# Kernel tuning notes

Hardware: AMD Instinct MI355X
Metric: run time of the kernel (lower is better)

## Reference

```python
import jax, jax.numpy as jnp
import numpy as np

B, N, Q, M, OUT = 8192, 512, 6, 1024, 256
QUANTILE_COEFFS = np.array([-3.0, -0.834, -0.248, 0.248, 0.834], dtype=np.float32)


def setup_inputs() -> dict:
    key = jax.random.key(0)
    k1, k2, k3, k4, k5, k6, k7 = jax.random.split(key, 7)
    x = jax.random.normal(k1, (B, N), dtype=jnp.float32)
    beta = jnp.zeros((N,), dtype=jnp.float32)
    gamma = jnp.ones((N,), dtype=jnp.float32)
    w = jax.random.normal(k2, (N * Q + M, OUT), dtype=jnp.float32)
    biases = jax.random.normal(k3, (1,), dtype=jnp.float32)
    # chosen_index rows: (count, n1, q1, n2, q2); n-indices in [0,N), q-indices in [0,Q)
    cnt = jnp.arange(M, dtype=jnp.int64)[:, None]
    n1 = jax.random.randint(k4, (M, 1), 0, N)
    q1 = jax.random.randint(k5, (M, 1), 0, Q)
    n2 = jax.random.randint(k6, (M, 1), 0, N)
    q2 = jax.random.randint(k7, (M, 1), 0, Q)
    chosen_index = jnp.concatenate([cnt, n1, q1, n2, q2], axis=1).astype(jnp.int64)
    return {"x": x, "beta": beta, "gamma": gamma, "w": w, "biases": biases,
            "chosen_index": chosen_index}


def reference(x, beta, gamma, w, biases, chosen_index):
    # Batch norm (EMA with decay=0.5 after register+update collapses to batch stats)
    mean = jnp.mean(x, axis=0)                      # (N,)
    var = jnp.var(x, axis=0)                        # (N,) biased, like unbiased=False
    normed = gamma * (x - mean) / jnp.sqrt(var + 0.001) + beta   # (B, N)
    # Maxout: base ReLU + 5 quantile-thresholded branches
    coeffs = jnp.asarray(QUANTILE_COEFFS)           # (5,)
    quant = coeffs[:, None] * var[None, :] + mean[None, :]       # (5, N)
    base = jnp.maximum(0.0, normed)[None]                        # (1, B, N)
    branches = jnp.maximum(0.0, normed[None] - quant[:, None, :] * gamma + beta)  # (5, B, N)
    stacked = jnp.concatenate([base, branches], axis=0)          # (Q, B, N)
    max_x = jnp.transpose(stacked, (1, 2, 0))                    # (B, N, Q)
    # Minout (test mode): per-row gather of two (n,q) coords, elementwise min
    n1, q1 = chosen_index[:, 1], chosen_index[:, 2]
    n2, q2 = chosen_index[:, 3], chosen_index[:, 4]
    D1 = max_x[:, n1, q1]                                        # (B, M)
    D2 = max_x[:, n2, q2]                                        # (B, M)
    min_x = jnp.minimum(D1, D2)                                  # (B, M)
    feat = jnp.concatenate([max_x.reshape(x.shape[0], -1), min_x], axis=1)  # (B, N*Q+M)
    output = feat @ w + biases                                   # (B, OUT)
    return output
```

## Files before the change

kernel.cpp:

```cpp
#include <hip/hip_runtime.h>
#include <stdint.h>

typedef unsigned int uint32;
typedef unsigned short u16;
typedef __attribute__((ext_vector_type(8))) short bf16x8;
typedef __attribute__((ext_vector_type(4))) float f32x4;

#define WS_SCALE 0
#define WS_SHIFT 512
#define WS_SUBQ  1024
#define WS_SHSUB 4096
#define WS_PSUM  8192
#define WS_PSQ   (8192+65536)
#define WRT_OFF  (1u<<20)
#define AMIN_OFF (3u<<20)
#define PART_OFF (19u<<20)

__device__ __forceinline__ u16 f2bf(float f){
  uint32 u; __builtin_memcpy(&u,&f,4);
  u = u + 0x7fffu + ((u>>16)&1u);
  return (u16)(u>>16);
}
__device__ __forceinline__ float bf2f(u16 b){
  uint32 u = ((uint32)b)<<16; float f; __builtin_memcpy(&f,&u,4); return f;
}
__device__ __forceinline__ uint32 pk2(float a, float b){
  return (uint32)f2bf(a) | ((uint32)f2bf(b)<<16);
}
__device__ __forceinline__ void gll16(u16* lds, const u16* g){
  __builtin_amdgcn_global_load_lds((const __attribute__((address_space(1))) uint32*)g,
                                   (__attribute__((address_space(3))) uint32*)lds, 16, 0, 0);
}

__global__ __launch_bounds__(512) void k_pre(const float* __restrict__ x,
                                             const float* __restrict__ w,
                                             float* __restrict__ ws,
                                             u16* __restrict__ wrT){
  int b = blockIdx.x, t = threadIdx.x;
  if (b < 128){
    const float* xp = x + (size_t)b*64*512 + t;
    float sum = 0.f, sq = 0.f;
    #pragma unroll 8
    for (int r=0; r<64; ++r){ float v = xp[(size_t)r*512]; sum += v; sq += v*v; }
    ws[WS_PSUM + b*512 + t] = sum;
    ws[WS_PSQ  + b*512 + t] = sq;
  } else {
    int c2 = b - 128;
    int o = t & 255, half = t >> 8;
    int swzrow = (o >> 1) & 3;
    u16* dst = wrT + (size_t)c2*8192 + o*32;
    #pragma unroll
    for (int gi=0; gi<2; ++gi){
      int g = half*2 + gi;
      union { bf16x8 v; u16 h[8]; } R;
      #pragma unroll
      for (int e=0; e<8; ++e){
        int k = g*8 + e;
        int sk;
        if (c2 < 96) sk = ((c2 & 15)*32 + k)*6 + (c2 >> 4);
        else         sk = 3072 + (c2 - 96)*32 + k;
        R.h[e] = f2bf(w[(size_t)sk*256 + o]);
      }
      *(bf16x8*)(dst + ((g ^ swzrow)*8)) = R.v;
    }
  }
}

__global__ __launch_bounds__(512) void k_stats_final(const float* __restrict__ beta,
                                                     const float* __restrict__ gamma,
                                                     float* __restrict__ ws){
  int n = threadIdx.x;
  float sum = 0.f, sq = 0.f;
  #pragma unroll 8
  for (int s2=0; s2<128; ++s2){ sum += ws[WS_PSUM + s2*512 + n]; sq += ws[WS_PSQ + s2*512 + n]; }
  float mean = sum * (1.0f/8192.0f);
  float var  = sq  * (1.0f/8192.0f) - mean*mean;
  float g = gamma[n], b = beta[n];
  float inv = 1.0f / sqrtf(var + 0.001f);
  float scale = g * inv;
  float shift = b - mean*scale;
  ws[WS_SCALE + n] = scale;
  ws[WS_SHIFT + n] = shift;
  const float QC[5] = {-3.0f, -0.834f, -0.248f, 0.248f, 0.834f};
  ws[WS_SUBQ  + n] = 0.f;
  ws[WS_SHSUB + n] = shift;
  #pragma unroll
  for (int c=0; c<5; ++c){
    float sub = (QC[c]*var + mean)*g - b;
    ws[WS_SUBQ  + (c+1)*512 + n] = sub;
    ws[WS_SHSUB + (c+1)*512 + n] = shift - sub;
  }
}

__global__ __launch_bounds__(256) void k_minfeat(const float* __restrict__ x,
                                                 const float* __restrict__ ws,
                                                 const int* __restrict__ ci,
                                                 u16* __restrict__ amin){
  __shared__ float nrm[8][512];
  __shared__ uint32 tnn[1024];
  __shared__ float ts1[1024];
  __shared__ float ts2[1024];
  int t = threadIdx.x;
  int b0 = blockIdx.x * 8;
  #pragma unroll
  for (int ii=0; ii<4; ++ii){
    int i = ii*256 + t;
    int n1 = ci[i*5+1], q1 = ci[i*5+2], n2 = ci[i*5+3], q2 = ci[i*5+4];
    tnn[i] = (uint32)n1 | ((uint32)n2 << 16);
    ts1[i] = ws[WS_SUBQ + q1*512 + n1];
    ts2[i] = ws[WS_SUBQ + q2*512 + n2];
  }
  {
    int r = t >> 5, c0 = (t & 31) * 16;
    const float* xr = x + (size_t)(b0 + r)*512 + c0;
    #pragma unroll
    for (int j=0;j<4;++j){
      float4 v  = *(const float4*)(xr + j*4);
      float4 sc = *(const float4*)(ws + WS_SCALE + c0 + j*4);
      float4 sh = *(const float4*)(ws + WS_SHIFT + c0 + j*4);
      float4 o; o.x=fmaf(v.x,sc.x,sh.x); o.y=fmaf(v.y,sc.y,sh.y);
      o.z=fmaf(v.z,sc.z,sh.z); o.w=fmaf(v.w,sc.w,sh.w);
      *(float4*)(&nrm[r][c0+j*4]) = o;
    }
  }
  __syncthreads();
  int m0 = t*4;
  uint4  nn = *(const uint4*)(&tnn[m0]);
  float4 s1 = *(const float4*)(&ts1[m0]);
  float4 s2 = *(const float4*)(&ts2[m0]);
  int cc = m0 >> 5, k = m0 & 31, g2 = k >> 3;
  #pragma unroll
  for (int r=0;r<8;++r){
    float v0 = fminf(fmaxf(nrm[r][nn.x & 0xffff] - s1.x, 0.f), fmaxf(nrm[r][nn.x >> 16] - s2.x, 0.f));
    float v1 = fminf(fmaxf(nrm[r][nn.y & 0xffff] - s1.y, 0.f), fmaxf(nrm[r][nn.y >> 16] - s2.y, 0.f));
    float v2 = fminf(fmaxf(nrm[r][nn.z & 0xffff] - s1.z, 0.f), fmaxf(nrm[r][nn.z >> 16] - s2.z, 0.f));
    float v3 = fminf(fmaxf(nrm[r][nn.w & 0xffff] - s1.w, 0.f), fmaxf(nrm[r][nn.w >> 16] - s2.w, 0.f));
    int pos = cc*32 + ((g2 ^ (((b0 + r) >> 1) & 3))*8) + (k & 7);
    uint2 pv; pv.x = pk2(v0,v1); pv.y = pk2(v2,v3);
    *(uint2*)(amin + (size_t)(b0 + r)*1024 + pos) = pv;
  }
}

__global__ __launch_bounds__(512,4) void k_gemm(const float* __restrict__ x,
                                                const float* __restrict__ ws,
                                                const u16* __restrict__ wrT,
                                                const u16* __restrict__ amin,
                                                u16* __restrict__ parts){
  __shared__ u16 wt[2][8192];
  __shared__ u16 ft[2][4096];
  __shared__ float pscale[512];
  __shared__ float pshsub[512];

  int t = threadIdx.x;
  int d = blockIdx.x;
  int mtile = d & 63, s = d >> 6;
  int brow = mtile * 128;
  bool isMin = (s >= 6);

  if (!isMin){
    pscale[t] = ws[WS_SCALE + t];
    pshsub[t] = ws[WS_SHSUB + s*512 + t];
  }

  int row = t >> 2, g = t & 3;
  int ftw = row*32 + ((g ^ ((row >> 1) & 3))*8);
  int wuni = t & ~63;
  const float* xrow = x + (size_t)(brow + row)*512;
  const u16* aminrow = amin + (size_t)(brow + row)*1024 + (isMin ? (s-6)*512 : 0) + g*8;
  const u16* wbase = wrT + (size_t)(s*16)*8192;

  int lane = t & 63, wv = t >> 6;
  int wm = wv >> 2, wn = wv & 3;
  int lr = lane & 15, lk = lane >> 4;
  int g16 = (lk ^ ((lr >> 1) & 3)) * 8;
  f32x4 acc[4][4] = {};

  __syncthreads();

  auto stage = [&](int cc, int nb){
    const u16* wsrc = wbase + (size_t)cc*8192;
    gll16(&wt[nb][wuni*8], wsrc + (size_t)t*8);
    gll16(&wt[nb][4096 + wuni*8], wsrc + 4096 + (size_t)t*8);
    if (!isMin){
      int col = cc*32 + g*8;
      float4 a0  = *(const float4*)(xrow + col);
      float4 a1  = *(const float4*)(xrow + col + 4);
      float4 sc0 = *(const float4*)(pscale + col);
      float4 sc1 = *(const float4*)(pscale + col + 4);
      float4 h0  = *(const float4*)(pshsub + col);
      float4 h1  = *(const float4*)(pshsub + col + 4);
      union { bf16x8 v; uint32 u[4]; } R;
      R.u[0] = pk2(fmaxf(fmaf(a0.x,sc0.x,h0.x),0.f), fmaxf(fmaf(a0.y,sc0.y,h0.y),0.f));
      R.u[1] = pk2(fmaxf(fmaf(a0.z,sc0.z,h0.z),0.f), fmaxf(fmaf(a0.w,sc0.w,h0.w),0.f));
      R.u[2] = pk2(fmaxf(fmaf(a1.x,sc1.x,h1.x),0.f), fmaxf(fmaf(a1.y,sc1.y,h1.y),0.f));
      R.u[3] = pk2(fmaxf(fmaf(a1.z,sc1.z,h1.z),0.f), fmaxf(fmaf(a1.w,sc1.w,h1.w),0.f));
      *(bf16x8*)(&ft[nb][ftw]) = R.v;
    } else {
      gll16(&ft[nb][wuni*8], aminrow + cc*32);
    }
  };

  auto compute = [&](int cb){
    bf16x8 A[4], Bv[4];
    #pragma unroll
    for (int mi=0; mi<4; ++mi)
      A[mi] = *(const bf16x8*)(&ft[cb][(wm*64 + mi*16 + lr)*32 + g16]);
    #pragma unroll
    for (int ni=0; ni<4; ++ni)
      Bv[ni] = *(const bf16x8*)(&wt[cb][(wn*64 + ni*16 + lr)*32 + g16]);
    #pragma unroll
    for (int mi=0; mi<4; ++mi)
      #pragma unroll
      for (int ni=0; ni<4; ++ni)
        acc[mi][ni] = __builtin_amdgcn_mfma_f32_16x16x32_bf16(A[mi], Bv[ni], acc[mi][ni], 0, 0, 0);
  };

  stage(0, 0);
  __syncthreads();
  int cur = 0;
  for (int c=0; c<16; ++c){
    if (c < 15) stage(c+1, cur^1);
    compute(cur);
    __syncthreads();
    cur ^= 1;
  }

  u16* pp = parts + ((size_t)s*8192 + brow)*256;
  #pragma unroll
  for (int mi=0; mi<4; ++mi)
    #pragma unroll
    for (int ni=0; ni<4; ++ni)
      #pragma unroll
      for (int r=0; r<4; ++r){
        int rl = wm*64 + mi*16 + lk*4 + r;
        int cl = wn*64 + ni*16 + lr;
        pp[(size_t)rl*256 + cl] = f2bf(acc[mi][ni][r]);
      }
}

__global__ __launch_bounds__(256) void k_reduce(const u16* __restrict__ parts,
                                                const float* __restrict__ biases,
                                                float* __restrict__ out){
  int i = (blockIdx.x*256 + threadIdx.x) * 8;
  float b = biases[0];
  float a[8];
  #pragma unroll
  for (int j=0;j<8;++j) a[j] = b;
  #pragma unroll
  for (int s2=0;s2<8;++s2){
    bf16x8 v = *(const bf16x8*)(parts + (size_t)s2*2097152 + i);
    #pragma unroll
    for (int j=0;j<8;++j) a[j] += bf2f((u16)v[j]);
  }
  float4 o0 = {a[0],a[1],a[2],a[3]}, o1 = {a[4],a[5],a[6],a[7]};
  *(float4*)(out + i) = o0;
  *(float4*)(out + i + 4) = o1;
}

extern "C" void kernel_launch(void* const* d_in, const int* in_sizes, int n_in,
                              void* d_out, int out_size, void* d_ws, size_t ws_size,
                              hipStream_t stream){
  const float* x      = (const float*)d_in[0];
  const float* beta   = (const float*)d_in[1];
  const float* gamma  = (const float*)d_in[2];
  const float* w      = (const float*)d_in[3];
  const float* biases = (const float*)d_in[4];
  const int*   ci     = (const int*)d_in[5];
  float* out = (float*)d_out;
  float* wsf = (float*)d_ws;
  u16* wrT   = (u16*)((char*)d_ws + WRT_OFF);
  u16* amin  = (u16*)((char*)d_ws + AMIN_OFF);
  u16* parts = (u16*)((char*)d_ws + PART_OFF);

  k_pre         <<<256, 512, 0, stream>>>(x, w, wsf, wrT);
  k_stats_final <<<1,   512, 0, stream>>>(beta, gamma, wsf);
  k_minfeat     <<<1024,256, 0, stream>>>(x, wsf, ci, amin);
  k_gemm        <<<512, 512, 0, stream>>>(x, wsf, wrT, amin, parts);
  k_reduce      <<<1024,256, 0, stream>>>(parts, biases, out);
}
```

Measured before the change: 61.99 us.

## Precompute bf16 normalized x, load GEMM A operands directly to registers

k_minfeat now also writes the normalized activations as bf16 to a workspace buffer. The GEMM reads its A fragments straight from global memory into registers, subtracts the per-branch bf16 quantile offset and applies ReLU there, which removes the A-tile LDS staging and the fp32 x reads. Separately, the stats reduction gets more partial blocks in k_pre and a 16-block two-level final reduction instead of one block. The trade-off is an extra bf16 write and read of the normalized x, uncoalesced 16-byte per-lane global loads in the GEMM inner loop, and extra rounding because the subtraction happens after bf16 quantization.

```diff
diff --git a/kernel.cpp b/kernel.cpp
--- a/kernel.cpp
+++ b/kernel.cpp
@@ -1,4 +1,5 @@
 #include <hip/hip_runtime.h>
+#include <hip/hip_bf16.h>
 #include <stdint.h>
 
 typedef unsigned int uint32;
@@ -9,12 +10,13 @@
 #define WS_SCALE 0
 #define WS_SHIFT 512
 #define WS_SUBQ  1024
-#define WS_SHSUB 4096
+#define WS_SUBQB 4096
 #define WS_PSUM  8192
-#define WS_PSQ   (8192+65536)
-#define WRT_OFF  (1u<<20)
-#define AMIN_OFF (3u<<20)
-#define PART_OFF (19u<<20)
+#define WS_PSQ   (8192+131072)
+#define WRT_OFF  (2u<<20)
+#define AMIN_OFF (4u<<20)
+#define PART_OFF (21u<<20)
+#define NRM_OFF  (54u<<20)
 
 __device__ __forceinline__ u16 f2bf(float f){
   uint32 u; __builtin_memcpy(&u,&f,4);
@@ -27,6 +29,8 @@
 __device__ __forceinline__ uint32 pk2(float a, float b){
   return (uint32)f2bf(a) | ((uint32)f2bf(b)<<16);
 }
+__device__ __forceinline__ float plo(uint32 p){ uint32 u=p<<16; float f; __builtin_memcpy(&f,&u,4); return f; }
+__device__ __forceinline__ float phi(uint32 p){ uint32 u=p&0xffff0000u; float f; __builtin_memcpy(&f,&u,4); return f; }
 __device__ __forceinline__ void gll16(u16* lds, const u16* g){
   __builtin_amdgcn_global_load_lds((const __attribute__((address_space(1))) uint32*)g,
                                    (__attribute__((address_space(3))) uint32*)lds, 16, 0, 0);
@@ -37,15 +41,15 @@
                                              float* __restrict__ ws,
                                              u16* __restrict__ wrT){
   int b = blockIdx.x, t = threadIdx.x;
-  if (b < 128){
-    const float* xp = x + (size_t)b*64*512 + t;
+  if (b < 256){
+    const float* xp = x + (size_t)b*32*512 + t;
     float sum = 0.f, sq = 0.f;
     #pragma unroll 8
-    for (int r=0; r<64; ++r){ float v = xp[(size_t)r*512]; sum += v; sq += v*v; }
+    for (int r=0; r<32; ++r){ float v = xp[(size_t)r*512]; sum += v; sq += v*v; }
     ws[WS_PSUM + b*512 + t] = sum;
     ws[WS_PSQ  + b*512 + t] = sq;
   } else {
-    int c2 = b - 128;
+    int c2 = b - 256;
     int o = t & 255, half = t >> 8;
     int swzrow = (o >> 1) & 3;
     u16* dst = wrT + (size_t)c2*8192 + o*32;
@@ -69,33 +73,48 @@
 __global__ __launch_bounds__(512) void k_stats_final(const float* __restrict__ beta,
                                                      const float* __restrict__ gamma,
                                                      float* __restrict__ ws){
-  int n = threadIdx.x;
-  float sum = 0.f, sq = 0.f;
-  #pragma unroll 8
-  for (int s2=0; s2<128; ++s2){ sum += ws[WS_PSUM + s2*512 + n]; sq += ws[WS_PSQ + s2*512 + n]; }
-  float mean = sum * (1.0f/8192.0f);
-  float var  = sq  * (1.0f/8192.0f) - mean*mean;
-  float g = gamma[n], b = beta[n];
-  float inv = 1.0f / sqrtf(var + 0.001f);
-  float scale = g * inv;
-  float shift = b - mean*scale;
-  ws[WS_SCALE + n] = scale;
-  ws[WS_SHIFT + n] = shift;
-  const float QC[5] = {-3.0f, -0.834f, -0.248f, 0.248f, 0.834f};
-  ws[WS_SUBQ  + n] = 0.f;
-  ws[WS_SHSUB + n] = shift;
-  #pragma unroll
-  for (int c=0; c<5; ++c){
-    float sub = (QC[c]*var + mean)*g - b;
-    ws[WS_SUBQ  + (c+1)*512 + n] = sub;
-    ws[WS_SHSUB + (c+1)*512 + n] = shift - sub;
+  __shared__ float rs[16][32], rq[16][32];
+  int t = threadIdx.x;
+  int nl = t & 31, sl = t >> 5;
+  int n = blockIdx.x*32 + nl;
+  float sum=0.f, sq=0.f;
+  #pragma unroll
+  for (int j=0;j<16;++j){
+    int p = sl*16 + j;
+    sum += ws[WS_PSUM + p*512 + n];
+    sq  += ws[WS_PSQ  + p*512 + n];
+  }
+  rs[sl][nl]=sum; rq[sl][nl]=sq;
+  __syncthreads();
+  if (sl==0){
+    #pragma unroll
+    for (int j=1;j<16;++j){ sum+=rs[j][nl]; sq+=rq[j][nl]; }
+    float mean = sum * (1.0f/8192.0f);
+    float var  = sq  * (1.0f/8192.0f) - mean*mean;
+    float g = gamma[n], b = beta[n];
+    float inv = 1.0f / sqrtf(var + 0.001f);
+    float scale = g * inv;
+    float shift = b - mean*scale;
+    ws[WS_SCALE + n] = scale;
+    ws[WS_SHIFT + n] = shift;
+    u16* subqb = (u16*)(ws + WS_SUBQB);
+    const float QC[5] = {-3.0f, -0.834f, -0.248f, 0.248f, 0.834f};
+    ws[WS_SUBQ + n] = 0.f;
+    subqb[n] = 0;
+    #pragma unroll
+    for (int c=0; c<5; ++c){
+      float sub = (QC[c]*var + mean)*g - b;
+      ws[WS_SUBQ + (c+1)*512 + n] = sub;
+      subqb[(c+1)*512 + n] = f2bf(sub);
+    }
   }
 }
 
 __global__ __launch_bounds__(256) void k_minfeat(const float* __restrict__ x,
                                                  const float* __restrict__ ws,
                                                  const int* __restrict__ ci,
-                                                 u16* __restrict__ amin){
+                                                 u16* __restrict__ amin,
+                                                 u16* __restrict__ nrmg){
   __shared__ float nrm[8][512];
   __shared__ uint32 tnn[1024];
   __shared__ float ts1[1024];
@@ -113,6 +132,7 @@
   {
     int r = t >> 5, c0 = (t & 31) * 16;
     const float* xr = x + (size_t)(b0 + r)*512 + c0;
+    u16* ng = nrmg + (size_t)(b0 + r)*512 + c0;
     #pragma unroll
     for (int j=0;j<4;++j){
       float4 v  = *(const float4*)(xr + j*4);
@@ -121,6 +141,8 @@
       float4 o; o.x=fmaf(v.x,sc.x,sh.x); o.y=fmaf(v.y,sc.y,sh.y);
       o.z=fmaf(v.z,sc.z,sh.z); o.w=fmaf(v.w,sc.w,sh.w);
       *(float4*)(&nrm[r][c0+j*4]) = o;
+      uint2 pv; pv.x = pk2(o.x,o.y); pv.y = pk2(o.z,o.w);
+      *(uint2*)(ng + j*4) = pv;
     }
   }
   __syncthreads();
@@ -128,28 +150,23 @@
   uint4  nn = *(const uint4*)(&tnn[m0]);
   float4 s1 = *(const float4*)(&ts1[m0]);
   float4 s2 = *(const float4*)(&ts2[m0]);
-  int cc = m0 >> 5, k = m0 & 31, g2 = k >> 3;
   #pragma unroll
   for (int r=0;r<8;++r){
     float v0 = fminf(fmaxf(nrm[r][nn.x & 0xffff] - s1.x, 0.f), fmaxf(nrm[r][nn.x >> 16] - s2.x, 0.f));
     float v1 = fminf(fmaxf(nrm[r][nn.y & 0xffff] - s1.y, 0.f), fmaxf(nrm[r][nn.y >> 16] - s2.y, 0.f));
     float v2 = fminf(fmaxf(nrm[r][nn.z & 0xffff] - s1.z, 0.f), fmaxf(nrm[r][nn.z >> 16] - s2.z, 0.f));
     float v3 = fminf(fmaxf(nrm[r][nn.w & 0xffff] - s1.w, 0.f), fmaxf(nrm[r][nn.w >> 16] - s2.w, 0.f));
-    int pos = cc*32 + ((g2 ^ (((b0 + r) >> 1) & 3))*8) + (k & 7);
     uint2 pv; pv.x = pk2(v0,v1); pv.y = pk2(v2,v3);
-    *(uint2*)(amin + (size_t)(b0 + r)*1024 + pos) = pv;
-  }
-}
-
-__global__ __launch_bounds__(512,4) void k_gemm(const float* __restrict__ x,
-                                                const float* __restrict__ ws,
+    *(uint2*)(amin + (size_t)(b0 + r)*1024 + m0) = pv;
+  }
+}
+
+__global__ __launch_bounds__(512,4) void k_gemm(const u16* __restrict__ nrmg,
+                                                const u16* __restrict__ ws16,
                                                 const u16* __restrict__ wrT,
                                                 const u16* __restrict__ amin,
                                                 u16* __restrict__ parts){
   __shared__ u16 wt[2][8192];
-  __shared__ u16 ft[2][4096];
-  __shared__ float pscale[512];
-  __shared__ float pshsub[512];
 
   int t = threadIdx.x;
   int d = blockIdx.x;
@@ -157,72 +174,77 @@
   int brow = mtile * 128;
   bool isMin = (s >= 6);
 
-  if (!isMin){
-    pscale[t] = ws[WS_SCALE + t];
-    pshsub[t] = ws[WS_SHSUB + s*512 + t];
-  }
-
-  int row = t >> 2, g = t & 3;
-  int ftw = row*32 + ((g ^ ((row >> 1) & 3))*8);
-  int wuni = t & ~63;
-  const float* xrow = x + (size_t)(brow + row)*512;
-  const u16* aminrow = amin + (size_t)(brow + row)*1024 + (isMin ? (s-6)*512 : 0) + g*8;
-  const u16* wbase = wrT + (size_t)(s*16)*8192;
-
   int lane = t & 63, wv = t >> 6;
   int wm = wv >> 2, wn = wv & 3;
   int lr = lane & 15, lk = lane >> 4;
-  int g16 = (lk ^ ((lr >> 1) & 3)) * 8;
+  int wuni = t & ~63;
+  const u16* wbase = wrT + (size_t)(s*16)*8192;
+
+  const u16* arow; int astr;
+  if (isMin){ arow = amin + (size_t)(brow + wm*64 + lr)*1024 + (s-6)*512; astr = 1024; }
+  else      { arow = nrmg + (size_t)(brow + wm*64 + lr)*512;              astr = 512;  }
+  const u16* subb = ws16 + s*512;
+
+  int osw[4];
+  #pragma unroll
+  for (int ni=0; ni<4; ++ni){
+    int o = wn*64 + ni*16 + lr;
+    osw[ni] = o*32 + ((lk ^ ((o>>1)&3))*8);
+  }
   f32x4 acc[4][4] = {};
-
-  __syncthreads();
-
-  auto stage = [&](int cc, int nb){
+  uint4 nv[4]; uint4 sb;
+
+  auto wstage = [&](int cc){
     const u16* wsrc = wbase + (size_t)cc*8192;
+    int nb = cc & 1;
     gll16(&wt[nb][wuni*8], wsrc + (size_t)t*8);
     gll16(&wt[nb][4096 + wuni*8], wsrc + 4096 + (size_t)t*8);
-    if (!isMin){
-      int col = cc*32 + g*8;
-      float4 a0  = *(const float4*)(xrow + col);
-      float4 a1  = *(const float4*)(xrow + col + 4);
-      float4 sc0 = *(const float4*)(pscale + col);
-      float4 sc1 = *(const float4*)(pscale + col + 4);
-      float4 h0  = *(const float4*)(pshsub + col);
-      float4 h1  = *(const float4*)(pshsub + col + 4);
-      union { bf16x8 v; uint32 u[4]; } R;
-      R.u[0] = pk2(fmaxf(fmaf(a0.x,sc0.x,h0.x),0.f), fmaxf(fmaf(a0.y,sc0.y,h0.y),0.f));
-      R.u[1] = pk2(fmaxf(fmaf(a0.z,sc0.z,h0.z),0.f), fmaxf(fmaf(a0.w,sc0.w,h0.w),0.f));
-      R.u[2] = pk2(fmaxf(fmaf(a1.x,sc1.x,h1.x),0.f), fmaxf(fmaf(a1.y,sc1.y,h1.y),0.f));
-      R.u[3] = pk2(fmaxf(fmaf(a1.z,sc1.z,h1.z),0.f), fmaxf(fmaf(a1.w,sc1.w,h1.w),0.f));
-      *(bf16x8*)(&ft[nb][ftw]) = R.v;
+  };
+  auto loadA = [&](int cc){
+    int co = cc*32 + lk*8;
+    #pragma unroll
+    for (int mi=0; mi<4; ++mi)
+      nv[mi] = *(const uint4*)(arow + (size_t)mi*16*astr + co);
+    if (!isMin) sb = *(const uint4*)(subb + co);
+  };
+  auto compute = [&](int cb){
+    union { bf16x8 v; uint4 q; } Af[4];
+    if (isMin){
+      #pragma unroll
+      for (int mi=0; mi<4; ++mi) Af[mi].q = nv[mi];
     } else {
-      gll16(&ft[nb][wuni*8], aminrow + cc*32);
+      #pragma unroll
+      for (int mi=0; mi<4; ++mi){
+        uint32 const* wq = (uint32 const*)&nv[mi];
+        uint32 const* sq = (uint32 const*)&sb;
+        union { bf16x8 v; uint32 u[4]; } R;
+        #pragma unroll
+        for (int j=0; j<4; ++j){
+          float a0 = fmaxf(plo(wq[j]) - plo(sq[j]), 0.f);
+          float a1 = fmaxf(phi(wq[j]) - phi(sq[j]), 0.f);
+          __hip_bfloat162 h = __float22bfloat162_rn(float2{a0,a1});
+          __builtin_memcpy(&R.u[j], &h, 4);
+        }
+        Af[mi].v = R.v;
+      }
+    }
+    #pragma unroll
+    for (int ni=0; ni<4; ++ni){
+      bf16x8 Bf = *(const bf16x8*)(&wt[cb][osw[ni]]);
+      #pragma unroll
+      for (int mi=0; mi<4; ++mi)
+        acc[mi][ni] = __builtin_amdgcn_mfma_f32_16x16x32_bf16(Af[mi].v, Bf, acc[mi][ni], 0, 0, 0);
     }
   };
 
-  auto compute = [&](int cb){
-    bf16x8 A[4], Bv[4];
-    #pragma unroll
-    for (int mi=0; mi<4; ++mi)
-      A[mi] = *(const bf16x8*)(&ft[cb][(wm*64 + mi*16 + lr)*32 + g16]);
-    #pragma unroll
-    for (int ni=0; ni<4; ++ni)
-      Bv[ni] = *(const bf16x8*)(&wt[cb][(wn*64 + ni*16 + lr)*32 + g16]);
-    #pragma unroll
-    for (int mi=0; mi<4; ++mi)
-      #pragma unroll
-      for (int ni=0; ni<4; ++ni)
-        acc[mi][ni] = __builtin_amdgcn_mfma_f32_16x16x32_bf16(A[mi], Bv[ni], acc[mi][ni], 0, 0, 0);
-  };
-
-  stage(0, 0);
+  loadA(0);
+  wstage(0);
   __syncthreads();
-  int cur = 0;
   for (int c=0; c<16; ++c){
-    if (c < 15) stage(c+1, cur^1);
-    compute(cur);
+    if (c < 15) wstage(c+1);
+    compute(c & 1);
+    if (c < 15) loadA(c+1);
     __syncthreads();
-    cur ^= 1;
   }
 
   u16* pp = parts + ((size_t)s*8192 + brow)*256;
@@ -271,10 +293,12 @@
   u16* wrT   = (u16*)((char*)d_ws + WRT_OFF);
   u16* amin  = (u16*)((char*)d_ws + AMIN_OFF);
   u16* parts = (u16*)((char*)d_ws + PART_OFF);
-
-  k_pre         <<<256, 512, 0, stream>>>(x, w, wsf, wrT);
-  k_stats_final <<<1,   512, 0, stream>>>(beta, gamma, wsf);
-  k_minfeat     <<<1024,256, 0, stream>>>(x, wsf, ci, amin);
-  k_gemm        <<<512, 512, 0, stream>>>(x, wsf, wrT, amin, parts);
+  u16* nrmg  = (u16*)((char*)d_ws + NRM_OFF);
+  const u16* subqb = (const u16*)(wsf + WS_SUBQB);
+
+  k_pre         <<<384, 512, 0, stream>>>(x, w, wsf, wrT);
+  k_stats_final <<<16,  512, 0, stream>>>(beta, gamma, wsf);
+  k_minfeat     <<<1024,256, 0, stream>>>(x, wsf, ci, amin, nrmg);
+  k_gemm        <<<512, 512, 0, stream>>>(nrmg, subqb, wrT, amin, parts);
   k_reduce      <<<1024,256, 0, stream>>>(parts, biases, out);
 }
```

New measurement: 98.19 us. 58.4% more time.

## Prefetch x two chunks ahead in GEMM and parallelize stats reduction

Applied to the files above, without the earlier changes.

The GEMM main loop now loads raw x values two K-chunks ahead into a register double buffer, then normalizes and packs them to LDS one chunk ahead, so global-load latency is hidden behind MFMA work. The column-statistics pass is split across twice as many blocks with half the rows each. The final stats kernel now uses 16 blocks with a shared-memory tree reduction instead of a single block running a serial loop. This costs extra registers in the GEMM, which may lower occupancy, and twice as much partial-sum traffic in the workspace.

```diff
diff --git a/kernel.cpp b/kernel.cpp
--- a/kernel.cpp
+++ b/kernel.cpp
@@ -11,10 +11,10 @@
 #define WS_SUBQ  1024
 #define WS_SHSUB 4096
 #define WS_PSUM  8192
-#define WS_PSQ   (8192+65536)
-#define WRT_OFF  (1u<<20)
-#define AMIN_OFF (3u<<20)
-#define PART_OFF (19u<<20)
+#define WS_PSQ   (8192+131072)
+#define WRT_OFF  (2u<<20)
+#define AMIN_OFF (4u<<20)
+#define PART_OFF (21u<<20)
 
 __device__ __forceinline__ u16 f2bf(float f){
   uint32 u; __builtin_memcpy(&u,&f,4);
@@ -37,15 +37,15 @@
                                              float* __restrict__ ws,
                                              u16* __restrict__ wrT){
   int b = blockIdx.x, t = threadIdx.x;
-  if (b < 128){
-    const float* xp = x + (size_t)b*64*512 + t;
+  if (b < 256){
+    const float* xp = x + (size_t)b*32*512 + t;
     float sum = 0.f, sq = 0.f;
     #pragma unroll 8
-    for (int r=0; r<64; ++r){ float v = xp[(size_t)r*512]; sum += v; sq += v*v; }
+    for (int r=0; r<32; ++r){ float v = xp[(size_t)r*512]; sum += v; sq += v*v; }
     ws[WS_PSUM + b*512 + t] = sum;
     ws[WS_PSQ  + b*512 + t] = sq;
   } else {
-    int c2 = b - 128;
+    int c2 = b - 256;
     int o = t & 255, half = t >> 8;
     int swzrow = (o >> 1) & 3;
     u16* dst = wrT + (size_t)c2*8192 + o*32;
@@ -69,26 +69,39 @@
 __global__ __launch_bounds__(512) void k_stats_final(const float* __restrict__ beta,
                                                      const float* __restrict__ gamma,
                                                      float* __restrict__ ws){
-  int n = threadIdx.x;
-  float sum = 0.f, sq = 0.f;
-  #pragma unroll 8
-  for (int s2=0; s2<128; ++s2){ sum += ws[WS_PSUM + s2*512 + n]; sq += ws[WS_PSQ + s2*512 + n]; }
-  float mean = sum * (1.0f/8192.0f);
-  float var  = sq  * (1.0f/8192.0f) - mean*mean;
-  float g = gamma[n], b = beta[n];
-  float inv = 1.0f / sqrtf(var + 0.001f);
-  float scale = g * inv;
-  float shift = b - mean*scale;
-  ws[WS_SCALE + n] = scale;
-  ws[WS_SHIFT + n] = shift;
-  const float QC[5] = {-3.0f, -0.834f, -0.248f, 0.248f, 0.834f};
-  ws[WS_SUBQ  + n] = 0.f;
-  ws[WS_SHSUB + n] = shift;
-  #pragma unroll
-  for (int c=0; c<5; ++c){
-    float sub = (QC[c]*var + mean)*g - b;
-    ws[WS_SUBQ  + (c+1)*512 + n] = sub;
-    ws[WS_SHSUB + (c+1)*512 + n] = shift - sub;
+  __shared__ float rs[16][32], rq[16][32];
+  int t = threadIdx.x;
+  int nl = t & 31, sl = t >> 5;
+  int n = blockIdx.x*32 + nl;
+  float sum=0.f, sq=0.f;
+  #pragma unroll
+  for (int j=0;j<16;++j){
+    int p = sl*16 + j;
+    sum += ws[WS_PSUM + p*512 + n];
+    sq  += ws[WS_PSQ  + p*512 + n];
+  }
+  rs[sl][nl]=sum; rq[sl][nl]=sq;
+  __syncthreads();
+  if (sl==0){
+    #pragma unroll
+    for (int j=1;j<16;++j){ sum+=rs[j][nl]; sq+=rq[j][nl]; }
+    float mean = sum * (1.0f/8192.0f);
+    float var  = sq  * (1.0f/8192.0f) - mean*mean;
+    float g = gamma[n], b = beta[n];
+    float inv = 1.0f / sqrtf(var + 0.001f);
+    float scale = g * inv;
+    float shift = b - mean*scale;
+    ws[WS_SCALE + n] = scale;
+    ws[WS_SHIFT + n] = shift;
+    const float QC[5] = {-3.0f, -0.834f, -0.248f, 0.248f, 0.834f};
+    ws[WS_SUBQ  + n] = 0.f;
+    ws[WS_SHSUB + n] = shift;
+    #pragma unroll
+    for (int c=0; c<5; ++c){
+      float sub = (QC[c]*var + mean)*g - b;
+      ws[WS_SUBQ  + (c+1)*512 + n] = sub;
+      ws[WS_SHSUB + (c+1)*512 + n] = shift - sub;
+    }
   }
 }
 
@@ -174,32 +187,33 @@
   int lr = lane & 15, lk = lane >> 4;
   int g16 = (lk ^ ((lr >> 1) & 3)) * 8;
   f32x4 acc[4][4] = {};
-
-  __syncthreads();
-
-  auto stage = [&](int cc, int nb){
+  float4 xa[2][2];
+
+  auto loadX = [&](int cc, int xb){
+    int col = cc*32 + g*8;
+    xa[xb][0] = *(const float4*)(xrow + col);
+    xa[xb][1] = *(const float4*)(xrow + col + 4);
+  };
+  auto stageW = [&](int cc, int nb){
     const u16* wsrc = wbase + (size_t)cc*8192;
     gll16(&wt[nb][wuni*8], wsrc + (size_t)t*8);
     gll16(&wt[nb][4096 + wuni*8], wsrc + 4096 + (size_t)t*8);
-    if (!isMin){
-      int col = cc*32 + g*8;
-      float4 a0  = *(const float4*)(xrow + col);
-      float4 a1  = *(const float4*)(xrow + col + 4);
-      float4 sc0 = *(const float4*)(pscale + col);
-      float4 sc1 = *(const float4*)(pscale + col + 4);
-      float4 h0  = *(const float4*)(pshsub + col);
-      float4 h1  = *(const float4*)(pshsub + col + 4);
-      union { bf16x8 v; uint32 u[4]; } R;
-      R.u[0] = pk2(fmaxf(fmaf(a0.x,sc0.x,h0.x),0.f), fmaxf(fmaf(a0.y,sc0.y,h0.y),0.f));
-      R.u[1] = pk2(fmaxf(fmaf(a0.z,sc0.z,h0.z),0.f), fmaxf(fmaf(a0.w,sc0.w,h0.w),0.f));
-      R.u[2] = pk2(fmaxf(fmaf(a1.x,sc1.x,h1.x),0.f), fmaxf(fmaf(a1.y,sc1.y,h1.y),0.f));
-      R.u[3] = pk2(fmaxf(fmaf(a1.z,sc1.z,h1.z),0.f), fmaxf(fmaf(a1.w,sc1.w,h1.w),0.f));
-      *(bf16x8*)(&ft[nb][ftw]) = R.v;
-    } else {
-      gll16(&ft[nb][wuni*8], aminrow + cc*32);
-    }
+    if (isMin) gll16(&ft[nb][wuni*8], aminrow + cc*32);
   };
-
+  auto packFT = [&](int cc, int nb, int xb){
+    int col = cc*32 + g*8;
+    float4 a0 = xa[xb][0], a1 = xa[xb][1];
+    float4 sc0 = *(const float4*)(pscale + col);
+    float4 sc1 = *(const float4*)(pscale + col + 4);
+    float4 h0  = *(const float4*)(pshsub + col);
+    float4 h1  = *(const float4*)(pshsub + col + 4);
+    union { bf16x8 v; uint32 u[4]; } R;
+    R.u[0] = pk2(fmaxf(fmaf(a0.x,sc0.x,h0.x),0.f), fmaxf(fmaf(a0.y,sc0.y,h0.y),0.f));
+    R.u[1] = pk2(fmaxf(fmaf(a0.z,sc0.z,h0.z),0.f), fmaxf(fmaf(a0.w,sc0.w,h0.w),0.f));
+    R.u[2] = pk2(fmaxf(fmaf(a1.x,sc1.x,h1.x),0.f), fmaxf(fmaf(a1.y,sc1.y,h1.y),0.f));
+    R.u[3] = pk2(fmaxf(fmaf(a1.z,sc1.z,h1.z),0.f), fmaxf(fmaf(a1.w,sc1.w,h1.w),0.f));
+    *(bf16x8*)(&ft[nb][ftw]) = R.v;
+  };
   auto compute = [&](int cb){
     bf16x8 A[4], Bv[4];
     #pragma unroll
@@ -215,11 +229,19 @@
         acc[mi][ni] = __builtin_amdgcn_mfma_f32_16x16x32_bf16(A[mi], Bv[ni], acc[mi][ni], 0, 0, 0);
   };
 
-  stage(0, 0);
   __syncthreads();
+  if (!isMin) loadX(0, 0);
+  stageW(0, 0);
+  if (!isMin){ packFT(0, 0, 0); loadX(1, 1); }
+  __syncthreads();
+
   int cur = 0;
   for (int c=0; c<16; ++c){
-    if (c < 15) stage(c+1, cur^1);
+    if (!isMin && c < 14) loadX(c+2, c & 1);
+    if (c < 15){
+      stageW(c+1, cur^1);
+      if (!isMin) packFT(c+1, cur^1, (c+1) & 1);
+    }
     compute(cur);
     __syncthreads();
     cur ^= 1;
@@ -272,8 +294,8 @@
   u16* amin  = (u16*)((char*)d_ws + AMIN_OFF);
   u16* parts = (u16*)((char*)d_ws + PART_OFF);
 
-  k_pre         <<<256, 512, 0, stream>>>(x, w, wsf, wrT);
-  k_stats_final <<<1,   512, 0, stream>>>(beta, gamma, wsf);
+  k_pre         <<<384, 512, 0, stream>>>(x, w, wsf, wrT);
+  k_stats_final <<<16,  512, 0, stream>>>(beta, gamma, wsf);
   k_minfeat     <<<1024,256, 0, stream>>>(x, wsf, ci, amin);
   k_gemm        <<<512, 512, 0, stream>>>(x, wsf, wrT, amin, parts);
   k_reduce      <<<1024,256, 0, stream>>>(parts, biases, out);
```

Measured after the change: 54.55 us. 12.0% less time.
